# Optimization experiments

Measured on AMD Instinct MI355X. Metric: run time of the kernel, lower is better.

The kernel has to match this reference:

```python
import jax, jax.numpy as jnp
import numpy as np

N, L, C, S = 4096, 512, 16, 32


def setup_inputs() -> dict:
    key = jax.random.key(0)
    k1, k2, k3, k4 = jax.random.split(key, 4)
    raw = jax.random.normal(k1, (N, L, C), dtype=jnp.float32)
    # valid log-probs: logsumexp along C is slightly < 0
    log_input_probs = jax.nn.log_softmax(raw, axis=-1) - 0.01
    return {
        "log_input_probs": log_input_probs,
        "logit_initial_state_probs": jax.random.normal(k2, (S,), dtype=jnp.float32),
        "logit_transition_probs": jax.random.normal(k3, (S, C, S), dtype=jnp.float32),
        "logit_accepting_state_probs": jax.random.normal(k4, (S,), dtype=jnp.float32),
    }


def reference(log_input_probs, logit_initial_state_probs, logit_transition_probs,
              logit_accepting_state_probs):
    initial_state_probs = jax.nn.softmax(logit_initial_state_probs, axis=0)          # (S,)
    transition_probs = jax.nn.softmax(logit_transition_probs, axis=2)                # (S,C,S)
    accepting_log = jax.nn.log_sigmoid(logit_accepting_state_probs)                  # (S,)
    input_probs = jnp.exp(log_input_probs)                                           # (N,L,C)

    n = log_input_probs.shape[0]
    p0 = jnp.broadcast_to(initial_state_probs[None, :], (n, initial_state_probs.shape[0]))

    def step(p_state, x_t):
        # p_state: (N,S) prev-state probs; x_t: (N,C) symbol probs at step t
        p_new = jnp.einsum('bp,bc,pcn->bn', p_state, x_t, transition_probs)
        return p_new, None

    xs = jnp.swapaxes(input_probs, 0, 1)  # (L,N,C) for scan over time
    p_final, _ = jax.lax.scan(step, p0, xs)

    log_p_state = jnp.log(p_final + 1e-20)                                           # (N,S)
    log_acceptance = jax.nn.logsumexp(log_p_state + accepting_log[None, :], axis=1)  # (N,)
    return log_acceptance[None]  # (1,N)
```

## Files before the change

### kernel.cpp

```cpp
#include <hip/hip_runtime.h>
#include <math.h>

typedef _Float16 f16;
typedef _Float16 f16x2 __attribute__((ext_vector_type(2)));
typedef _Float16 f16x4 __attribute__((ext_vector_type(4)));
typedef _Float16 f16x8 __attribute__((ext_vector_type(8)));
typedef float    f32x4 __attribute__((ext_vector_type(4)));

#define NB 4096
#define LT 512
#define NC 16
#define NS 32

#define WS_P0     0
#define WS_SIG    128
#define WS_SUMSIG 256
#define WS_FWDT   512
#define WS_BWDT   (512 + 32768)
#define WS_F      (512 + 65536)
#define WS_G      (WS_F + 32*4096*4)

#if __has_builtin(__builtin_amdgcn_exp2f)
#define EXP2F __builtin_amdgcn_exp2f
#else
#define EXP2F exp2f
#endif

__global__ __launch_bounds__(512) void pdfa_prep(const float* __restrict__ tlogit,
                                                 const float* __restrict__ ilogit,
                                                 const float* __restrict__ alogit,
                                                 char* __restrict__ ws) {
    int tid = threadIdx.x;
    f16* fwdT = (f16*)(ws + WS_FWDT);
    f16* bwdT = (f16*)(ws + WS_BWDT);
    int p = tid >> 4, c = tid & 15;
    const float* row = tlogit + p * 512 + c * 32;
    float mx = row[0];
    for (int n = 1; n < 32; ++n) mx = fmaxf(mx, row[n]);
    float s = 0.f;
    for (int n = 0; n < 32; ++n) s += expf(row[n] - mx);
    float inv = 1.f / s;
    for (int n = 0; n < 32; ++n) {
        float tv = expf(row[n] - mx) * inv;
        {
            int q = (p & 15) >> 2, j = (p & 3) + 4 * (p >> 4);
            int r = n >> 4, m = n & 15;
            fwdT[((c * 2 + r) * 64 + 16 * q + m) * 8 + j] = (f16)tv;
        }
        {
            int q = (n & 15) >> 2, j = (n & 3) + 4 * (n >> 4);
            int r = p >> 4, m = p & 15;
            bwdT[((c * 2 + r) * 64 + 16 * q + m) * 8 + j] = (f16)tv;
        }
    }
    if (tid < 32) {
        float m0 = ilogit[0];
        for (int n = 1; n < 32; ++n) m0 = fmaxf(m0, ilogit[n]);
        float s0 = 0.f;
        for (int n = 0; n < 32; ++n) s0 += expf(ilogit[n] - m0);
        ((float*)(ws + WS_P0))[tid]  = 256.f * expf(ilogit[tid] - m0) / s0;
        ((float*)(ws + WS_SIG))[tid] = 256.f / (1.f + expf(-alogit[tid]));
    }
    if (tid == 0) {
        float ss = 0.f;
        for (int n = 0; n < 32; ++n) ss += 1.f / (1.f + expf(-alogit[n]));
        *(float*)(ws + WS_SUMSIG) = ss;
    }
}

#define EC(v) ((f16)EXP2F((v) * 1.44269504089f))

__global__ __launch_bounds__(64, 1) void pdfa_main(const float* __restrict__ login,
                                                   char* __restrict__ ws) {
    const int lane = threadIdx.x;
    const int q    = lane >> 4;
    const int col  = lane & 15;
    const int bid  = blockIdx.x;
    const int dir  = bid & 1;
    const int b0   = (bid >> 1) << 4;

    const char* tblb = ws + (dir ? WS_BWDT : WS_FWDT);
    f16x8 af[16][2];
#pragma unroll
    for (int kc = 0; kc < 16; ++kc)
#pragma unroll
        for (int r = 0; r < 2; ++r)
            af[kc][r] = *(const f16x8*)(tblb + ((kc * 2 + r) * 64 + lane) * 16);

    const float* initv = (const float*)(ws + (dir ? WS_SIG : WS_P0));
    f32x4 pr0, pr1;
#pragma unroll
    for (int j = 0; j < 4; ++j) { pr0[j] = initv[4 * q + j]; pr1[j] = initv[16 + 4 * q + j]; }
    f16x8 pvec = {(f16)pr0[0], (f16)pr0[1], (f16)pr0[2], (f16)pr0[3],
                  (f16)pr1[0], (f16)pr1[1], (f16)pr1[2], (f16)pr1[3]};

    const float* xg = login + (size_t)(b0 + col) * (LT * NC);
    const f32x4 z4{};
    f32x4 rn[4];
    f16x8 xq0, xq1;

#define TT(S)  (dir ? (511 - (S)) : (S))
#define TTC(S) TT((((S) > 511) ? 511 : (S)))
    {
        const f32x4* sp = (const f32x4*)(xg + (size_t)TT(0) * NC);
        f32x4 r0 = sp[0], r1 = sp[1], r2 = sp[2], r3 = sp[3];
        xq0 = f16x8{EC(r0[0]), EC(r0[1]), EC(r0[2]), EC(r0[3]),
                    EC(r1[0]), EC(r1[1]), EC(r1[2]), EC(r1[3])};
        xq1 = f16x8{EC(r2[0]), EC(r2[1]), EC(r2[2]), EC(r2[3]),
                    EC(r3[0]), EC(r3[1]), EC(r3[2]), EC(r3[3])};
        const f32x4* sp1 = (const f32x4*)(xg + (size_t)TT(1) * NC);
        rn[0] = sp1[0]; rn[1] = sp1[1]; rn[2] = sp1[2]; rn[3] = sp1[3];
    }

    for (int s = 0; s < 256; ++s) {
        f32x4 a0[4], a1[4];
        __builtin_amdgcn_s_setprio(1);
#pragma unroll
        for (int kc = 0; kc < 16; ++kc) {
            f16 xs = (kc < 8) ? xq0[kc & 7] : xq1[kc & 7];
            f16x8 bs = {xs, xs, xs, xs, xs, xs, xs, xs};
            f16x8 bf = pvec * bs;
            if (kc < 4) {
                a0[kc & 3] = __builtin_amdgcn_mfma_f32_16x16x32_f16(af[kc][0], bf, z4, 0, 0, 0);
                a1[kc & 3] = __builtin_amdgcn_mfma_f32_16x16x32_f16(af[kc][1], bf, z4, 0, 0, 0);
            } else {
                a0[kc & 3] = __builtin_amdgcn_mfma_f32_16x16x32_f16(af[kc][0], bf, a0[kc & 3], 0, 0, 0);
                a1[kc & 3] = __builtin_amdgcn_mfma_f32_16x16x32_f16(af[kc][1], bf, a1[kc & 3], 0, 0, 0);
            }
        }
        __builtin_amdgcn_s_setprio(0);

        f16x8 xn0 = f16x8{EC(rn[0][0]), EC(rn[0][1]), EC(rn[0][2]), EC(rn[0][3]),
                          EC(rn[1][0]), EC(rn[1][1]), EC(rn[1][2]), EC(rn[1][3])};
        f16x8 xn1 = f16x8{EC(rn[2][0]), EC(rn[2][1]), EC(rn[2][2]), EC(rn[2][3]),
                          EC(rn[3][0]), EC(rn[3][1]), EC(rn[3][2]), EC(rn[3][3])};
        {
            const f32x4* sp = (const f32x4*)(xg + (size_t)TTC(s + 2) * NC);
            rn[0] = sp[0]; rn[1] = sp[1]; rn[2] = sp[2]; rn[3] = sp[3];
        }

        pr0 = (a0[0] + a0[1]) + (a0[2] + a0[3]);
        pr1 = (a1[0] + a1[1]) + (a1[2] + a1[3]);
        pvec = f16x8{(f16)pr0[0], (f16)pr0[1], (f16)pr0[2], (f16)pr0[3],
                     (f16)pr1[0], (f16)pr1[1], (f16)pr1[2], (f16)pr1[3]};
        xq0 = xn0; xq1 = xn1;
    }
#undef TT
#undef TTC

    float* outv = (float*)(ws + (dir ? WS_G : WS_F));
#pragma unroll
    for (int j = 0; j < 4; ++j) {
        outv[(size_t)(4 * q + j) * NB + b0 + col]      = pr0[j];
        outv[(size_t)(16 + 4 * q + j) * NB + b0 + col] = pr1[j];
    }
}

__global__ __launch_bounds__(256) void pdfa_combine(const char* __restrict__ ws,
                                                    float* __restrict__ out) {
    int b = blockIdx.x * 256 + threadIdx.x;
    const float* f = (const float*)(ws + WS_F);
    const float* g = (const float*)(ws + WS_G);
    float ss = *(const float*)(ws + WS_SUMSIG);
    float dot = 0.f;
#pragma unroll
    for (int s2 = 0; s2 < 32; ++s2)
        dot = fmaf(f[s2 * NB + b], g[s2 * NB + b], dot);
    out[b] = logf(dot * (1.f / 65536.f) + 1e-20f * ss);
}

extern "C" void kernel_launch(void* const* d_in, const int* in_sizes, int n_in,
                              void* d_out, int out_size, void* d_ws, size_t ws_size,
                              hipStream_t stream) {
    const float* login = (const float*)d_in[0];
    const float* ilog  = (const float*)d_in[1];
    const float* tlog  = (const float*)d_in[2];
    const float* alog  = (const float*)d_in[3];
    char* ws = (char*)d_ws;

    pdfa_prep<<<1, 512, 0, stream>>>(tlog, ilog, alog, ws);
    pdfa_main<<<512, 64, 0, stream>>>(login, ws);
    pdfa_combine<<<NB / 256, 256, 0, stream>>>(ws, (float*)d_out);
}
```

Before: 175.9 us.

## Split each recurrence step across two waves with LDS partial-sum exchange

Each block now runs two wavefronts that each own half of the previous-state dimension, halving the MFMA chain per wave on the serial time recurrence. Partial state vectors are exchanged through double-buffered shared memory with a barrier every step, and the symbol probabilities are loaded cooperatively and staged in LDS. The transition tables are re-laid out in the prep kernel to match the per-wave split. This trades a shorter per-step dependency chain and lower register pressure for a block barrier plus LDS round trip on every time step. The partial sums are added in fp16.

```diff
diff --git a/kernel.cpp b/kernel.cpp
--- a/kernel.cpp
+++ b/kernel.cpp
@@ -5,6 +5,7 @@
 typedef _Float16 f16x2 __attribute__((ext_vector_type(2)));
 typedef _Float16 f16x4 __attribute__((ext_vector_type(4)));
 typedef _Float16 f16x8 __attribute__((ext_vector_type(8)));
+typedef float    f32x2 __attribute__((ext_vector_type(2)));
 typedef float    f32x4 __attribute__((ext_vector_type(4)));
 
 #define NB 4096
@@ -43,14 +44,16 @@
     for (int n = 0; n < 32; ++n) {
         float tv = expf(row[n] - mx) * inv;
         {
-            int q = (p & 15) >> 2, j = (p & 3) + 4 * (p >> 4);
-            int r = n >> 4, m = n & 15;
-            fwdT[((c * 2 + r) * 64 + 16 * q + m) * 8 + j] = (f16)tv;
+            int w = p >> 4, q = (p >> 2) & 3, kc = c >> 1, r = n >> 4;
+            int lane = q * 16 + (n & 15);
+            int j = (p & 3) + 4 * (c & 1);
+            fwdT[(((w * 8 + kc) * 2 + r) * 64 + lane) * 8 + j] = (f16)tv;
         }
         {
-            int q = (n & 15) >> 2, j = (n & 3) + 4 * (n >> 4);
-            int r = p >> 4, m = p & 15;
-            bwdT[((c * 2 + r) * 64 + 16 * q + m) * 8 + j] = (f16)tv;
+            int w = n >> 4, q = (n >> 2) & 3, kc = c >> 1, r = p >> 4;
+            int lane = q * 16 + (p & 15);
+            int j = (n & 3) + 4 * (c & 1);
+            bwdT[(((w * 8 + kc) * 2 + r) * 64 + lane) * 8 + j] = (f16)tv;
         }
     }
     if (tid < 32) {
@@ -70,9 +73,15 @@
 
 #define EC(v) ((f16)EXP2F((v) * 1.44269504089f))
 
-__global__ __launch_bounds__(64, 1) void pdfa_main(const float* __restrict__ login,
-                                                   char* __restrict__ ws) {
-    const int lane = threadIdx.x;
+#define XOFF 4096
+#define XB   640
+
+__global__ __launch_bounds__(128, 2) void pdfa_main(const float* __restrict__ login,
+                                                    char* __restrict__ ws) {
+    __shared__ __align__(16) char lds[4096 + 2 * XB];
+    const int tid  = threadIdx.x;
+    const int w    = tid >> 6;
+    const int lane = tid & 63;
     const int q    = lane >> 4;
     const int col  = lane & 15;
     const int bid  = blockIdx.x;
@@ -80,79 +89,87 @@
     const int b0   = (bid >> 1) << 4;
 
     const char* tblb = ws + (dir ? WS_BWDT : WS_FWDT);
-    f16x8 af[16][2];
-#pragma unroll
-    for (int kc = 0; kc < 16; ++kc)
+    f16x8 af[8][2];
+#pragma unroll
+    for (int kc = 0; kc < 8; ++kc)
 #pragma unroll
         for (int r = 0; r < 2; ++r)
-            af[kc][r] = *(const f16x8*)(tblb + ((kc * 2 + r) * 64 + lane) * 16);
+            af[kc][r] = *(const f16x8*)(tblb + (((w * 8 + kc) * 2 + r) * 64 + lane) * 16);
 
     const float* initv = (const float*)(ws + (dir ? WS_SIG : WS_P0));
-    f32x4 pr0, pr1;
-#pragma unroll
-    for (int j = 0; j < 4; ++j) { pr0[j] = initv[4 * q + j]; pr1[j] = initv[16 + 4 * q + j]; }
-    f16x8 pvec = {(f16)pr0[0], (f16)pr0[1], (f16)pr0[2], (f16)pr0[3],
-                  (f16)pr1[0], (f16)pr1[1], (f16)pr1[2], (f16)pr1[3]};
-
-    const float* xg = login + (size_t)(b0 + col) * (LT * NC);
+    f16x8 pnew;
+#pragma unroll
+    for (int jj = 0; jj < 8; ++jj)
+        pnew[jj] = (f16)initv[4 * q + (jj & 3) + 16 * (jj >> 2)];
+
+    const int pcol = tid >> 3, cp = tid & 7;
+    const float* xg = login + (size_t)(b0 + pcol) * (LT * NC) + 2 * cp;
+    char* xw = lds + XOFF + pcol * 40 + cp * 4;
+    const char* xr = lds + XOFF + col * 40;
+
+    char* pw = lds + (w * 64 + lane) * 16;
+    const char* prd = lds + ((1 - w) * 64 + lane) * 16;
+
     const f32x4 z4{};
-    f32x4 rn[4];
-    f16x8 xq0, xq1;
+    f32x2 rb;
 
 #define TT(S)  (dir ? (511 - (S)) : (S))
 #define TTC(S) TT((((S) > 511) ? 511 : (S)))
     {
-        const f32x4* sp = (const f32x4*)(xg + (size_t)TT(0) * NC);
-        f32x4 r0 = sp[0], r1 = sp[1], r2 = sp[2], r3 = sp[3];
-        xq0 = f16x8{EC(r0[0]), EC(r0[1]), EC(r0[2]), EC(r0[3]),
-                    EC(r1[0]), EC(r1[1]), EC(r1[2]), EC(r1[3])};
-        xq1 = f16x8{EC(r2[0]), EC(r2[1]), EC(r2[2]), EC(r2[3]),
-                    EC(r3[0]), EC(r3[1]), EC(r3[2]), EC(r3[3])};
-        const f32x4* sp1 = (const f32x4*)(xg + (size_t)TT(1) * NC);
-        rn[0] = sp1[0]; rn[1] = sp1[1]; rn[2] = sp1[2]; rn[3] = sp1[3];
-    }
+        f32x2 r0 = *(const f32x2*)(xg + (size_t)TT(0) * NC);
+        *(f16x2*)(xw) = f16x2{EC(r0[0]), EC(r0[1])};
+        rb = *(const f32x2*)(xg + (size_t)TT(1) * NC);
+    }
+    __syncthreads();
+    f16x8 xqlo = *(const f16x8*)(xr);
+    f16x8 xqhi = *(const f16x8*)(xr + 16);
 
     for (int s = 0; s < 256; ++s) {
+        const int ph = s & 1;
+        f16x4 phh = w ? f16x4{pnew[4], pnew[5], pnew[6], pnew[7]}
+                      : f16x4{pnew[0], pnew[1], pnew[2], pnew[3]};
         f32x4 a0[4], a1[4];
         __builtin_amdgcn_s_setprio(1);
 #pragma unroll
-        for (int kc = 0; kc < 16; ++kc) {
-            f16 xs = (kc < 8) ? xq0[kc & 7] : xq1[kc & 7];
-            f16x8 bs = {xs, xs, xs, xs, xs, xs, xs, xs};
-            f16x8 bf = pvec * bs;
+        for (int kc = 0; kc < 8; ++kc) {
+            f16 xa = (kc < 4) ? xqlo[2 * kc]     : xqhi[2 * (kc - 4)];
+            f16 xb = (kc < 4) ? xqlo[2 * kc + 1] : xqhi[2 * (kc - 4) + 1];
+            f16x8 bf = {phh[0] * xa, phh[1] * xa, phh[2] * xa, phh[3] * xa,
+                        phh[0] * xb, phh[1] * xb, phh[2] * xb, phh[3] * xb};
             if (kc < 4) {
-                a0[kc & 3] = __builtin_amdgcn_mfma_f32_16x16x32_f16(af[kc][0], bf, z4, 0, 0, 0);
-                a1[kc & 3] = __builtin_amdgcn_mfma_f32_16x16x32_f16(af[kc][1], bf, z4, 0, 0, 0);
+                a0[kc] = __builtin_amdgcn_mfma_f32_16x16x32_f16(af[kc][0], bf, z4, 0, 0, 0);
+                a1[kc] = __builtin_amdgcn_mfma_f32_16x16x32_f16(af[kc][1], bf, z4, 0, 0, 0);
             } else {
-                a0[kc & 3] = __builtin_amdgcn_mfma_f32_16x16x32_f16(af[kc][0], bf, a0[kc & 3], 0, 0, 0);
-                a1[kc & 3] = __builtin_amdgcn_mfma_f32_16x16x32_f16(af[kc][1], bf, a1[kc & 3], 0, 0, 0);
+                a0[kc - 4] = __builtin_amdgcn_mfma_f32_16x16x32_f16(af[kc][0], bf, a0[kc - 4], 0, 0, 0);
+                a1[kc - 4] = __builtin_amdgcn_mfma_f32_16x16x32_f16(af[kc][1], bf, a1[kc - 4], 0, 0, 0);
             }
         }
         __builtin_amdgcn_s_setprio(0);
 
-        f16x8 xn0 = f16x8{EC(rn[0][0]), EC(rn[0][1]), EC(rn[0][2]), EC(rn[0][3]),
-                          EC(rn[1][0]), EC(rn[1][1]), EC(rn[1][2]), EC(rn[1][3])};
-        f16x8 xn1 = f16x8{EC(rn[2][0]), EC(rn[2][1]), EC(rn[2][2]), EC(rn[2][3]),
-                          EC(rn[3][0]), EC(rn[3][1]), EC(rn[3][2]), EC(rn[3][3])};
-        {
-            const f32x4* sp = (const f32x4*)(xg + (size_t)TTC(s + 2) * NC);
-            rn[0] = sp[0]; rn[1] = sp[1]; rn[2] = sp[2]; rn[3] = sp[3];
-        }
-
-        pr0 = (a0[0] + a0[1]) + (a0[2] + a0[3]);
-        pr1 = (a1[0] + a1[1]) + (a1[2] + a1[3]);
-        pvec = f16x8{(f16)pr0[0], (f16)pr0[1], (f16)pr0[2], (f16)pr0[3],
-                     (f16)pr1[0], (f16)pr1[1], (f16)pr1[2], (f16)pr1[3]};
-        xq0 = xn0; xq1 = xn1;
+        *(f16x2*)(xw + (ph ^ 1) * XB) = f16x2{EC(rb[0]), EC(rb[1])};
+        rb = *(const f32x2*)(xg + (size_t)TTC(s + 2) * NC);
+
+        f32x4 pr0 = (a0[0] + a0[1]) + (a0[2] + a0[3]);
+        f32x4 pr1 = (a1[0] + a1[1]) + (a1[2] + a1[3]);
+        f16x8 mine = {(f16)pr0[0], (f16)pr0[1], (f16)pr0[2], (f16)pr0[3],
+                      (f16)pr1[0], (f16)pr1[1], (f16)pr1[2], (f16)pr1[3]};
+        *(f16x8*)(pw + ph * 2048) = mine;
+        __syncthreads();
+        f16x8 other = *(const f16x8*)(prd + ph * 2048);
+        xqlo = *(const f16x8*)(xr + (ph ^ 1) * XB);
+        xqhi = *(const f16x8*)(xr + (ph ^ 1) * XB + 16);
+        pnew = mine + other;
     }
 #undef TT
 #undef TTC
 
-    float* outv = (float*)(ws + (dir ? WS_G : WS_F));
-#pragma unroll
-    for (int j = 0; j < 4; ++j) {
-        outv[(size_t)(4 * q + j) * NB + b0 + col]      = pr0[j];
-        outv[(size_t)(16 + 4 * q + j) * NB + b0 + col] = pr1[j];
+    if (w == 0) {
+        float* outv = (float*)(ws + (dir ? WS_G : WS_F));
+#pragma unroll
+        for (int i = 0; i < 4; ++i) {
+            outv[(size_t)(4 * q + i) * NB + b0 + col]      = (float)pnew[i];
+            outv[(size_t)(16 + 4 * q + i) * NB + b0 + col] = (float)pnew[4 + i];
+        }
     }
 }
 
@@ -179,6 +196,6 @@
     char* ws = (char*)d_ws;
 
     pdfa_prep<<<1, 512, 0, stream>>>(tlog, ilog, alog, ws);
-    pdfa_main<<<512, 64, 0, stream>>>(login, ws);
+    pdfa_main<<<512, 128, 0, stream>>>(login, ws);
     pdfa_combine<<<NB / 256, 256, 0, stream>>>(ws, (float*)d_out);
 }
```

Result: no change. 172.9 us (-1.7%).
